# Kernel tuning notes

Hardware: AMD Instinct MI355X
Metric: run time of the kernel (lower is better)

## Reference

```python
import jax, jax.numpy as jnp
import numpy as np

N_CLANS = 600   # rows of graph_fc.npy -> number of clan classes
MAX_F = 128     # max families per clan (padding size for stacked family heads)
B, L, D = 8192, 64, 256
NEG = -1e9      # mask value for padded family logits


def setup_inputs() -> dict:
    key = jax.random.key(0)
    k1, k2, k3, k4, k5, k6 = jax.random.split(key, 6)
    output = jax.random.normal(k1, (B, L, D), dtype=jnp.float32)
    fc = jax.random.randint(k2, (N_CLANS,), 1, MAX_F + 1)           # families per clan
    label_clan = jax.random.randint(k3, (B,), 0, N_CLANS)
    raw = jax.random.randint(k4, (B,), 0, MAX_F)
    label_family = raw % fc[label_clan]                              # valid family per sample
    W_clan = jax.random.normal(k5, (N_CLANS, D), dtype=jnp.float32) * 0.05
    b_clan = jnp.zeros((N_CLANS,), dtype=jnp.float32)
    W_fam = jax.random.normal(k6, (N_CLANS, MAX_F, D), dtype=jnp.float32) * 0.05
    b_fam = jnp.zeros((N_CLANS, MAX_F), dtype=jnp.float32)
    return {"output": output, "label_clan": label_clan, "label_family": label_family,
            "fc": fc, "W_clan": W_clan, "b_clan": b_clan, "W_fam": W_fam, "b_fam": b_fam}


def reference(output, label_clan, label_family, fc, W_clan, b_clan, W_fam, b_fam):
    x = output.mean(axis=1)                                          # [B, D]
    # clan CE loss (reduction='sum')
    logits_c = x @ W_clan.T + b_clan                                 # [B, N_CLANS]
    logp_c = jax.nn.log_softmax(logits_c, axis=-1)
    loss_clan = -jnp.take_along_axis(logp_c, label_clan[:, None], axis=1).sum()
    # routed per-sample family head: gather head weights by clan label
    Wg = W_fam[label_clan]                                           # [B, MAX_F, D]
    bg = b_fam[label_clan]                                           # [B, MAX_F]
    logits_f = jnp.einsum('bfd,bd->bf', Wg, x) + bg                  # [B, MAX_F]
    n_fam = fc[label_clan]                                           # [B]
    valid = jnp.arange(MAX_F)[None, :] < n_fam[:, None]              # mask padded families
    logits_f = jnp.where(valid, logits_f, NEG)
    logp_f = jax.nn.log_softmax(logits_f, axis=-1)
    nll = -jnp.take_along_axis(logp_f, label_family[:, None], axis=1)[:, 0]  # [B]
    active = n_fam > 1                                               # only clans with >1 family
    loss_family = jnp.where(active, nll, 0.0).sum()
    count = active.sum()
    loss = (loss_clan + loss_family) / (output.shape[0] + count)
    return loss
```

## Files before the change

### kernel.cpp

```cpp
#include <hip/hip_runtime.h>
#include <hip/hip_bf16.h>

#define B_SZ 8192
#define L_SZ 64
#define D_SZ 256
#define NC   600
#define MAXF 128
#define CAP  64

__global__ __launch_bounds__(256) void mean_kernel(const float* __restrict__ out,
                                                   float* __restrict__ x) {
    int gid = blockIdx.x * 256 + threadIdx.x;
    int b = gid >> 6, d4 = gid & 63;
    const float4* p = (const float4*)(out + (size_t)b * L_SZ * D_SZ) + d4;
    float4 acc = {0.f, 0.f, 0.f, 0.f};
#pragma unroll 8
    for (int l = 0; l < L_SZ; ++l) {
        float4 v = p[(size_t)l * (D_SZ / 4)];
        acc.x += v.x; acc.y += v.y; acc.z += v.z; acc.w += v.w;
    }
    const float s = 1.0f / 64.0f;
    acc.x *= s; acc.y *= s; acc.z *= s; acc.w *= s;
    ((float4*)(x + (size_t)b * D_SZ))[d4] = acc;
}

__global__ __launch_bounds__(256) void scatter_kernel(const int* __restrict__ label_clan,
                                                      const int* __restrict__ fc,
                                                      int* __restrict__ cnt,
                                                      int* __restrict__ list,
                                                      int* __restrict__ active_cnt) {
    int b = blockIdx.x * 256 + threadIdx.x;
    int cl = label_clan[b];
    int pos = atomicAdd(&cnt[cl], 1);
    if (pos < CAP) list[cl * CAP + pos] = b;
    int act = (fc[cl] > 1) ? 1 : 0;
    unsigned long long ball = __ballot(act);
    if ((threadIdx.x & 63) == 0) atomicAdd(active_cnt, (int)__popcll(ball));
}

#define BM 64
#define BN 64
#define BK 32
__global__ __launch_bounds__(256) void clan_gemm(const float* __restrict__ x,
                                                 const float* __restrict__ Wc,
                                                 const float* __restrict__ bc,
                                                 float* __restrict__ logits) {
    __shared__ float As[BM][BK + 4];
    __shared__ float Bs[BN][BK + 4];
    int t = threadIdx.x;
    int tx = t & 15, ty = t >> 4;
    int row0 = blockIdx.x * BM;
    int col0 = blockIdx.y * BN;
    float acc[4][4] = {};
    for (int k0 = 0; k0 < D_SZ; k0 += BK) {
#pragma unroll
        for (int q = t; q < BM * BK / 4; q += 256) {
            int r = q >> 3, c4 = q & 7;
            float4 v = *(const float4*)(x + (size_t)(row0 + r) * D_SZ + k0 + c4 * 4);
            *(float4*)&As[r][c4 * 4] = v;
        }
#pragma unroll
        for (int q = t; q < BN * BK / 4; q += 256) {
            int r = q >> 3, c4 = q & 7;
            int cl = col0 + r;
            float4 v = {0.f, 0.f, 0.f, 0.f};
            if (cl < NC) v = *(const float4*)(Wc + (size_t)cl * D_SZ + k0 + c4 * 4);
            *(float4*)&Bs[r][c4 * 4] = v;
        }
        __syncthreads();
#pragma unroll
        for (int kk = 0; kk < BK; kk += 4) {
            float4 a[4], bb[4];
#pragma unroll
            for (int i = 0; i < 4; ++i) a[i] = *(float4*)&As[ty * 4 + i][kk];
#pragma unroll
            for (int j = 0; j < 4; ++j) bb[j] = *(float4*)&Bs[tx * 4 + j][kk];
#pragma unroll
            for (int i = 0; i < 4; ++i)
#pragma unroll
                for (int j = 0; j < 4; ++j)
                    acc[i][j] += a[i].x * bb[j].x + a[i].y * bb[j].y +
                                 a[i].z * bb[j].z + a[i].w * bb[j].w;
        }
        __syncthreads();
    }
#pragma unroll
    for (int i = 0; i < 4; ++i) {
        int m = row0 + ty * 4 + i;
#pragma unroll
        for (int j = 0; j < 4; ++j) {
            int c = col0 + tx * 4 + j;
            if (c < NC) logits[(size_t)m * NC + c] = acc[i][j] + bc[c];
        }
    }
}

__global__ __launch_bounds__(256) void clan_loss(const float* __restrict__ logits,
                                                 const int* __restrict__ label_clan,
                                                 float* __restrict__ acc_loss) {
    int b = blockIdx.x;
    const float* row = logits + (size_t)b * NC;
    int t = threadIdx.x;
    __shared__ float sred[8];
    float m = -1e30f;
    for (int c = t; c < NC; c += 256) m = fmaxf(m, row[c]);
#pragma unroll
    for (int off = 32; off; off >>= 1) m = fmaxf(m, __shfl_down(m, off));
    if ((t & 63) == 0) sred[t >> 6] = m;
    __syncthreads();
    float bm = fmaxf(fmaxf(sred[0], sred[1]), fmaxf(sred[2], sred[3]));
    float s = 0.f;
    for (int c = t; c < NC; c += 256) s += __expf(row[c] - bm);
#pragma unroll
    for (int off = 32; off; off >>= 1) s += __shfl_down(s, off);
    if ((t & 63) == 0) sred[4 + (t >> 6)] = s;
    __syncthreads();
    if (t == 0) {
        float tot = sred[4] + sred[5] + sred[6] + sred[7];
        float loss = __logf(tot) + bm - row[label_clan[b]];
        atomicAdd(acc_loss, loss);
    }
}

#define CHUNK 16
__global__ __launch_bounds__(256) void family_kernel(const float* __restrict__ x,
                                                     const float* __restrict__ Wf,
                                                     const float* __restrict__ bf,
                                                     const int* __restrict__ fc,
                                                     const int* __restrict__ cnt,
                                                     const int* __restrict__ list,
                                                     const int* __restrict__ label_family,
                                                     float* __restrict__ acc_loss) {
    int clan = blockIdx.x;
    int nf = fc[clan];
    if (nf <= 1) return;
    int n = min(cnt[clan], CAP);
    if (n == 0) return;
    __shared__ float sx[CHUNK][D_SZ];
    __shared__ float slog[CHUNK][MAXF];
    __shared__ int sb[CHUNK];
    int t = threadIdx.x;
    int lane = t & 63, wid = t >> 6;
    const float* Wbase = Wf + (size_t)clan * MAXF * D_SZ;

    for (int s0 = 0; s0 < n; s0 += CHUNK) {
        int cn = min(CHUNK, n - s0);
        if (t < cn) sb[t] = list[clan * CAP + s0 + t];
        __syncthreads();
        for (int q = t; q < cn * (D_SZ / 4); q += 256) {
            int s = q >> 6, d4 = q & 63;
            ((float4*)sx[s])[d4] = ((const float4*)(x + (size_t)sb[s] * D_SZ))[d4];
        }
        __syncthreads();
        for (int f = wid; f < nf; f += 4) {
            float4 w = ((const float4*)(Wbase + (size_t)f * D_SZ))[lane];
            float bias = bf[clan * MAXF + f];
            for (int s = 0; s < cn; ++s) {
                float4 xv = ((float4*)sx[s])[lane];
                float p = w.x * xv.x + w.y * xv.y + w.z * xv.z + w.w * xv.w;
#pragma unroll
                for (int off = 32; off; off >>= 1) p += __shfl_down(p, off);
                if (lane == 0) slog[s][f] = p + bias;
            }
        }
        __syncthreads();
        float wave_loss = 0.f;
        for (int s = wid; s < cn; s += 4) {
            float v0 = (lane < nf) ? slog[s][lane] : -1e30f;
            float v1 = (lane + 64 < nf) ? slog[s][lane + 64] : -1e30f;
            float m = fmaxf(v0, v1);
#pragma unroll
            for (int off = 32; off; off >>= 1) m = fmaxf(m, __shfl_down(m, off));
            m = __shfl(m, 0);
            float e = 0.f;
            if (lane < nf) e += __expf(v0 - m);
            if (lane + 64 < nf) e += __expf(v1 - m);
#pragma unroll
            for (int off = 32; off; off >>= 1) e += __shfl_down(e, off);
            if (lane == 0) {
                int b = sb[s];
                int lf = label_family[b];
                wave_loss += __logf(e) + m - slog[s][lf];
            }
        }
        if (lane == 0 && wave_loss != 0.f) atomicAdd(acc_loss, wave_loss);
        __syncthreads();
    }
}

__global__ void finalize_kernel(const float* __restrict__ accs,
                                const int* __restrict__ active_cnt,
                                float* __restrict__ out) {
    out[0] = (accs[0] + accs[1]) / (8192.0f + (float)(*active_cnt));
}

extern "C" void kernel_launch(void* const* d_in, const int* in_sizes, int n_in,
                              void* d_out, int out_size, void* d_ws, size_t ws_size,
                              hipStream_t stream) {
    (void)in_sizes; (void)n_in; (void)out_size; (void)ws_size;
    const float* output       = (const float*)d_in[0];
    const int*   label_clan   = (const int*)d_in[1];
    const int*   label_family = (const int*)d_in[2];
    const int*   fc           = (const int*)d_in[3];
    const float* W_clan       = (const float*)d_in[4];
    const float* b_clan       = (const float*)d_in[5];
    const float* W_fam        = (const float*)d_in[6];
    const float* b_fam        = (const float*)d_in[7];
    float* out = (float*)d_out;

    char* ws = (char*)d_ws;
    const size_t OFF_X    = 0;
    const size_t OFF_LOG  = OFF_X + (size_t)B_SZ * D_SZ * 4;
    const size_t OFF_CNT  = OFF_LOG + (size_t)B_SZ * NC * 4;
    const size_t OFF_LIST = OFF_CNT + 2560;
    const size_t OFF_ACC  = OFF_LIST + (size_t)NC * CAP * 4;
    float* x      = (float*)(ws + OFF_X);
    float* logits = (float*)(ws + OFF_LOG);
    int*   cnt    = (int*)(ws + OFF_CNT);
    int*   list   = (int*)(ws + OFF_LIST);
    float* accs   = (float*)(ws + OFF_ACC);
    int*   act    = (int*)(ws + OFF_ACC + 8);

    hipMemsetAsync(ws + OFF_CNT, 0, 2560 + (size_t)NC * CAP * 4 + 16, stream);

    mean_kernel<<<B_SZ * D_SZ / 4 / 256, 256, 0, stream>>>(output, x);
    scatter_kernel<<<B_SZ / 256, 256, 0, stream>>>(label_clan, fc, cnt, list, act);
    dim3 gg(B_SZ / BM, (NC + BN - 1) / BN);
    clan_gemm<<<gg, 256, 0, stream>>>(x, W_clan, b_clan, logits);
    clan_loss<<<B_SZ, 256, 0, stream>>>(logits, label_clan, accs);
    family_kernel<<<NC, 256, 0, stream>>>(x, W_fam, b_fam, fc, cnt, list, label_family, accs + 1);
    finalize_kernel<<<1, 1, 0, stream>>>(accs, act, out);
}
```

Measured before the change: 1.101 ms.

## Fuse clan GEMM with online log-softmax loss and drop logits buffer

Replaces the separate clan GEMM and per-row loss kernels with one kernel. Each block holds 32 rows of x in shared memory, sweeps all clan columns in tiles of 64, and keeps a running max and sum-exp per row. This removes the write and re-read of the full logits matrix and one launch. It also shrinks the memset to skip the family list, and has the family kernel do one atomic per block instead of one per wave per chunk. In exchange, each block re-streams the whole W_clan matrix, and the grid is small with extra syncs per column tile.

```diff
diff --git a/kernel.cpp b/kernel.cpp
--- a/kernel.cpp
+++ b/kernel.cpp
@@ -38,87 +38,110 @@
     if ((threadIdx.x & 63) == 0) atomicAdd(active_cnt, (int)__popcll(ball));
 }
 
-#define BM 64
-#define BN 64
-#define BK 32
-__global__ __launch_bounds__(256) void clan_gemm(const float* __restrict__ x,
-                                                 const float* __restrict__ Wc,
-                                                 const float* __restrict__ bc,
-                                                 float* __restrict__ logits) {
-    __shared__ float As[BM][BK + 4];
-    __shared__ float Bs[BN][BK + 4];
+#define CBM 32
+__global__ __launch_bounds__(256) void clan_fused(const float* __restrict__ x,
+                                                  const float* __restrict__ Wc,
+                                                  const float* __restrict__ bc,
+                                                  const int* __restrict__ label_clan,
+                                                  float* __restrict__ acc_loss) {
+    __shared__ float As[CBM][260];
+    __shared__ float Bs[64][68];
+    __shared__ float redm[CBM][16];
+    __shared__ float mrow[CBM], srow[CBM], mnew[CBM], lablog[CBM];
+    __shared__ int   labc[CBM];
     int t = threadIdx.x;
     int tx = t & 15, ty = t >> 4;
-    int row0 = blockIdx.x * BM;
-    int col0 = blockIdx.y * BN;
-    float acc[4][4] = {};
-    for (int k0 = 0; k0 < D_SZ; k0 += BK) {
-#pragma unroll
-        for (int q = t; q < BM * BK / 4; q += 256) {
-            int r = q >> 3, c4 = q & 7;
-            float4 v = *(const float4*)(x + (size_t)(row0 + r) * D_SZ + k0 + c4 * 4);
-            *(float4*)&As[r][c4 * 4] = v;
-        }
-#pragma unroll
-        for (int q = t; q < BN * BK / 4; q += 256) {
-            int r = q >> 3, c4 = q & 7;
-            int cl = col0 + r;
-            float4 v = {0.f, 0.f, 0.f, 0.f};
-            if (cl < NC) v = *(const float4*)(Wc + (size_t)cl * D_SZ + k0 + c4 * 4);
-            *(float4*)&Bs[r][c4 * 4] = v;
-        }
-        __syncthreads();
-#pragma unroll
-        for (int kk = 0; kk < BK; kk += 4) {
-            float4 a[4], bb[4];
-#pragma unroll
-            for (int i = 0; i < 4; ++i) a[i] = *(float4*)&As[ty * 4 + i][kk];
-#pragma unroll
-            for (int j = 0; j < 4; ++j) bb[j] = *(float4*)&Bs[tx * 4 + j][kk];
-#pragma unroll
-            for (int i = 0; i < 4; ++i)
-#pragma unroll
-                for (int j = 0; j < 4; ++j)
-                    acc[i][j] += a[i].x * bb[j].x + a[i].y * bb[j].y +
-                                 a[i].z * bb[j].z + a[i].w * bb[j].w;
-        }
-        __syncthreads();
-    }
-#pragma unroll
-    for (int i = 0; i < 4; ++i) {
-        int m = row0 + ty * 4 + i;
-#pragma unroll
-        for (int j = 0; j < 4; ++j) {
-            int c = col0 + tx * 4 + j;
-            if (c < NC) logits[(size_t)m * NC + c] = acc[i][j] + bc[c];
-        }
-    }
-}
-
-__global__ __launch_bounds__(256) void clan_loss(const float* __restrict__ logits,
-                                                 const int* __restrict__ label_clan,
-                                                 float* __restrict__ acc_loss) {
-    int b = blockIdx.x;
-    const float* row = logits + (size_t)b * NC;
-    int t = threadIdx.x;
-    __shared__ float sred[8];
-    float m = -1e30f;
-    for (int c = t; c < NC; c += 256) m = fmaxf(m, row[c]);
-#pragma unroll
-    for (int off = 32; off; off >>= 1) m = fmaxf(m, __shfl_down(m, off));
-    if ((t & 63) == 0) sred[t >> 6] = m;
+    int row0 = blockIdx.x * CBM;
+
+#pragma unroll
+    for (int rep = 0; rep < 8; ++rep) {
+        int idx = t + rep * 256;
+        int r = idx >> 6, c4 = idx & 63;
+        *(float4*)&As[r][c4 * 4] = *(const float4*)(x + (size_t)(row0 + r) * D_SZ + c4 * 4);
+    }
+    if (t < CBM) {
+        mrow[t] = -1e30f; srow[t] = 0.f; lablog[t] = 0.f;
+        labc[t] = label_clan[row0 + t];
+    }
     __syncthreads();
-    float bm = fmaxf(fmaxf(sred[0], sred[1]), fmaxf(sred[2], sred[3]));
-    float s = 0.f;
-    for (int c = t; c < NC; c += 256) s += __expf(row[c] - bm);
-#pragma unroll
-    for (int off = 32; off; off >>= 1) s += __shfl_down(s, off);
-    if ((t & 63) == 0) sred[4 + (t >> 6)] = s;
+
+    for (int ct = 0; ct < 10; ++ct) {
+        int c0 = ct * 64;
+        float acc[2][4] = {};
+        for (int k0 = 0; k0 < D_SZ; k0 += 64) {
+            __syncthreads();
+#pragma unroll
+            for (int rep = 0; rep < 4; ++rep) {
+                int idx = t + rep * 256;
+                int col = idx >> 4, kq = idx & 15;
+                int c = c0 + col;
+                float4 v = {0.f, 0.f, 0.f, 0.f};
+                if (c < NC) v = *(const float4*)(Wc + (size_t)c * D_SZ + k0 + kq * 4);
+                *(float4*)&Bs[col][kq * 4] = v;
+            }
+            __syncthreads();
+#pragma unroll
+            for (int kk = 0; kk < 16; ++kk) {
+                float4 a0 = *(float4*)&As[ty][k0 + kk * 4];
+                float4 a1 = *(float4*)&As[ty + 16][k0 + kk * 4];
+                float4 b[4];
+#pragma unroll
+                for (int j = 0; j < 4; ++j) b[j] = *(float4*)&Bs[tx + 16 * j][kk * 4];
+#pragma unroll
+                for (int j = 0; j < 4; ++j) {
+                    acc[0][j] += a0.x * b[j].x + a0.y * b[j].y + a0.z * b[j].z + a0.w * b[j].w;
+                    acc[1][j] += a1.x * b[j].x + a1.y * b[j].y + a1.z * b[j].z + a1.w * b[j].w;
+                }
+            }
+        }
+        float lg[2][4];
+#pragma unroll
+        for (int i = 0; i < 2; ++i) {
+            int row = ty + 16 * i;
+#pragma unroll
+            for (int j = 0; j < 4; ++j) {
+                int c = c0 + tx + 16 * j;
+                float v = (c < NC) ? acc[i][j] + bc[c] : -1e30f;
+                lg[i][j] = v;
+                if (c < NC && c == labc[row]) lablog[row] = v;
+            }
+        }
+#pragma unroll
+        for (int i = 0; i < 2; ++i) {
+            int row = ty + 16 * i;
+            redm[row][tx] = fmaxf(fmaxf(lg[i][0], lg[i][1]), fmaxf(lg[i][2], lg[i][3]));
+        }
+        __syncthreads();
+        if (t < CBM) {
+            float tm = redm[t][0];
+#pragma unroll
+            for (int q = 1; q < 16; ++q) tm = fmaxf(tm, redm[t][q]);
+            mnew[t] = fmaxf(mrow[t], tm);
+        }
+        __syncthreads();
+#pragma unroll
+        for (int i = 0; i < 2; ++i) {
+            int row = ty + 16 * i;
+            float mn = mnew[row];
+            redm[row][tx] = __expf(lg[i][0] - mn) + __expf(lg[i][1] - mn)
+                          + __expf(lg[i][2] - mn) + __expf(lg[i][3] - mn);
+        }
+        __syncthreads();
+        if (t < CBM) {
+            float s = 0.f;
+#pragma unroll
+            for (int q = 0; q < 16; ++q) s += redm[t][q];
+            srow[t] = srow[t] * __expf(mrow[t] - mnew[t]) + s;
+            mrow[t] = mnew[t];
+        }
+    }
     __syncthreads();
-    if (t == 0) {
-        float tot = sred[4] + sred[5] + sred[6] + sred[7];
-        float loss = __logf(tot) + bm - row[label_clan[b]];
-        atomicAdd(acc_loss, loss);
+    if (t < 64) {
+        float loss = 0.f;
+        if (t < CBM) loss = __logf(srow[t]) + mrow[t] - lablog[t];
+#pragma unroll
+        for (int off = 16; off; off >>= 1) loss += __shfl_down(loss, off);
+        if (t == 0) atomicAdd(acc_loss, loss);
     }
 }
 
@@ -139,10 +162,12 @@
     __shared__ float sx[CHUNK][D_SZ];
     __shared__ float slog[CHUNK][MAXF];
     __shared__ int sb[CHUNK];
+    __shared__ float wl[4];
     int t = threadIdx.x;
     int lane = t & 63, wid = t >> 6;
     const float* Wbase = Wf + (size_t)clan * MAXF * D_SZ;
 
+    float wave_loss = 0.f;
     for (int s0 = 0; s0 < n; s0 += CHUNK) {
         int cn = min(CHUNK, n - s0);
         if (t < cn) sb[t] = list[clan * CAP + s0 + t];
@@ -164,7 +189,6 @@
             }
         }
         __syncthreads();
-        float wave_loss = 0.f;
         for (int s = wid; s < cn; s += 4) {
             float v0 = (lane < nf) ? slog[s][lane] : -1e30f;
             float v1 = (lane + 64 < nf) ? slog[s][lane + 64] : -1e30f;
@@ -183,8 +207,13 @@
                 wave_loss += __logf(e) + m - slog[s][lf];
             }
         }
-        if (lane == 0 && wave_loss != 0.f) atomicAdd(acc_loss, wave_loss);
-        __syncthreads();
+        __syncthreads();
+    }
+    if (lane == 0) wl[wid] = wave_loss;
+    __syncthreads();
+    if (t == 0) {
+        float v = wl[0] + wl[1] + wl[2] + wl[3];
+        if (v != 0.f) atomicAdd(acc_loss, v);
     }
 }
 
@@ -210,24 +239,20 @@
 
     char* ws = (char*)d_ws;
     const size_t OFF_X    = 0;
-    const size_t OFF_LOG  = OFF_X + (size_t)B_SZ * D_SZ * 4;
-    const size_t OFF_CNT  = OFF_LOG + (size_t)B_SZ * NC * 4;
-    const size_t OFF_LIST = OFF_CNT + 2560;
-    const size_t OFF_ACC  = OFF_LIST + (size_t)NC * CAP * 4;
+    const size_t OFF_CNT  = OFF_X + (size_t)B_SZ * D_SZ * 4;
+    const size_t OFF_ACC  = OFF_CNT + 2560;
+    const size_t OFF_LIST = OFF_ACC + 16;
     float* x      = (float*)(ws + OFF_X);
-    float* logits = (float*)(ws + OFF_LOG);
     int*   cnt    = (int*)(ws + OFF_CNT);
-    int*   list   = (int*)(ws + OFF_LIST);
     float* accs   = (float*)(ws + OFF_ACC);
     int*   act    = (int*)(ws + OFF_ACC + 8);
-
-    hipMemsetAsync(ws + OFF_CNT, 0, 2560 + (size_t)NC * CAP * 4 + 16, stream);
+    int*   list   = (int*)(ws + OFF_LIST);
+
+    hipMemsetAsync(ws + OFF_CNT, 0, 2560 + 16, stream);
 
     mean_kernel<<<B_SZ * D_SZ / 4 / 256, 256, 0, stream>>>(output, x);
     scatter_kernel<<<B_SZ / 256, 256, 0, stream>>>(label_clan, fc, cnt, list, act);
-    dim3 gg(B_SZ / BM, (NC + BN - 1) / BN);
-    clan_gemm<<<gg, 256, 0, stream>>>(x, W_clan, b_clan, logits);
-    clan_loss<<<B_SZ, 256, 0, stream>>>(logits, label_clan, accs);
+    clan_fused<<<B_SZ / CBM, 256, 0, stream>>>(x, W_clan, b_clan, label_clan, accs);
     family_kernel<<<NC, 256, 0, stream>>>(x, W_fam, b_fam, fc, cnt, list, label_family, accs + 1);
     finalize_kernel<<<1, 1, 0, stream>>>(accs, act, out);
 }
```

Result: faster. 1.067 ms (-3.1%).
